# Optimization experiments

Measured on AMD Instinct MI355X. Metric: run time of the kernel, lower is better.

## Reference

```python
import jax, jax.numpy as jnp
import numpy as np

N, IN_DIM, HID = 8192, 256, 128


def _glorot(key, shape):
    lim = float(np.sqrt(6.0 / (shape[0] + shape[1])))
    return jax.random.uniform(key, shape, jnp.float32, -lim, lim)


def setup_inputs() -> dict:
    key = jax.random.key(0)
    ks = jax.random.split(key, 16)
    return {
        "x": jax.random.normal(ks[0], (N, IN_DIM), jnp.float32),
        "XY_Adj": jnp.zeros((N, N), jnp.float32),  # unused: overwritten by Cos_Adj in forward
        "w0": _glorot(ks[1], (IN_DIM, HID)),
        "w1": _glorot(ks[2], (IN_DIM, HID)),
        "Wq1": _glorot(ks[3], (IN_DIM, HID)), "bq1": jnp.zeros((HID,), jnp.float32),
        "Wk1": _glorot(ks[4], (IN_DIM, HID)), "bk1": jnp.zeros((HID,), jnp.float32),
        "Wv1": _glorot(ks[5], (IN_DIM, HID)), "bv1": jnp.zeros((HID,), jnp.float32),
        "Ws1": _glorot(ks[6], (IN_DIM, HID)), "bs1": jnp.zeros((HID,), jnp.float32),
        "Wq4": _glorot(ks[7], (HID, IN_DIM)), "bq4": jnp.zeros((IN_DIM,), jnp.float32),
        "Wk4": _glorot(ks[8], (HID, IN_DIM)), "bk4": jnp.zeros((IN_DIM,), jnp.float32),
        "Wv4": _glorot(ks[9], (HID, IN_DIM)), "bv4": jnp.zeros((IN_DIM,), jnp.float32),
        "Ws4": _glorot(ks[10], (HID, IN_DIM)), "bs4": jnp.zeros((IN_DIM,), jnp.float32),
    }


def _cos_adj(x, w0, w1):
    # Dense cosine-similarity adjacency, as in Cos_Adj.forward
    theta = x @ w0  # [N, HID]
    phi = x @ w1    # [N, HID]
    tn = jnp.linalg.norm(theta, axis=1, keepdims=True)  # [N,1]
    pn = jnp.linalg.norm(phi, axis=1, keepdims=True)    # [N,1]
    return (theta @ phi.T) / (tn @ pn.T + 1e-20)        # [N,N]


def _tconv(h, Wq, bq, Wk, bk, Wv, bv, Ws, bs):
    # PyG TransformerConv (heads=1, root_weight=True) on the fully-connected
    # graph produced by coo_matrix(sim_graph) == dense all-pairs attention.
    q = h @ Wq + bq
    k = h @ Wk + bk
    v = h @ Wv + bv
    scale = 1.0 / np.sqrt(q.shape[-1])
    attn = jax.nn.softmax((q @ k.T) * scale, axis=-1)  # [N,N]
    return attn @ v + (h @ Ws + bs)


def reference(x, XY_Adj, w0, w1,
              Wq1, bq1, Wk1, bk1, Wv1, bv1, Ws1, bs1,
              Wq4, bq4, Wk4, bk4, Wv4, bv4, Ws4, bs4):
    # Adjacency values only define the edge set (all N^2 pairs nonzero for
    # generic inputs); TransformerConv recomputes attention coefficients.
    sim = _cos_adj(x, w0, w1)  # noqa: F841 (edge set = nonzeros = all pairs)
    h1 = jax.nn.elu(_tconv(x, Wq1, bq1, Wk1, bk1, Wv1, bv1, Ws1, bs1))
    out = _tconv(h1, Wq4, bq4, Wk4, bk4, Wv4, bv4, Ws4, bs4)
    return out
```

## Files before the change

kernel.cpp:

```cpp
#include <hip/hip_runtime.h>

#define N_ROWS 8192
#define IN_DIM 256
#define HID 128

typedef __attribute__((ext_vector_type(8))) short bf16x8;
typedef __attribute__((ext_vector_type(4))) float f32x4;

__device__ __forceinline__ unsigned short f2bf(float f) {
    union { float f; unsigned u; } v; v.f = f;
    unsigned r = (v.u + 0x7FFFu + ((v.u >> 16) & 1u)) >> 16;
    return (unsigned short)r;
}

__global__ void pack_weights(const float* __restrict__ W0, const float* __restrict__ W1,
                             const float* __restrict__ W2, const float* __restrict__ W3,
                             const float* __restrict__ b0, const float* __restrict__ b1,
                             const float* __restrict__ b2, const float* __restrict__ b3,
                             unsigned short* __restrict__ WT, float* __restrict__ B,
                             int K, int HO)
{
    int NT = 4 * HO;
    int idx = blockIdx.x * blockDim.x + threadIdx.x;
    if (idx < NT * K) {
        int n = idx / K, k = idx - n * K;
        int s = n / HO, sn = n - s * HO;
        const float* W = (s == 0) ? W0 : (s == 1) ? W1 : (s == 2) ? W2 : W3;
        WT[idx] = f2bf(W[k * HO + sn]);
    }
    if (idx < NT) {
        int s = idx / HO, sn = idx - s * HO;
        const float* b = (s == 0) ? b0 : (s == 1) ? b1 : (s == 2) ? b2 : b3;
        B[idx] = b[sn];
    }
}

__global__ void cast_x(const float* __restrict__ in, unsigned short* __restrict__ out, int n) {
    int i = blockIdx.x * blockDim.x + threadIdx.x;
    if (i < n) out[i] = f2bf(in[i]);
}

__global__ void transpose_bf16(const unsigned short* __restrict__ in,
                               unsigned short* __restrict__ out, int R, int C)
{
    __shared__ unsigned short t[32][33];
    const int tx = threadIdx.x, ty = threadIdx.y;
    const int r0 = blockIdx.y * 32, c0 = blockIdx.x * 32;
    #pragma unroll
    for (int j = 0; j < 32; j += 8)
        t[ty + j][tx] = in[(size_t)(r0 + ty + j) * C + c0 + tx];
    __syncthreads();
    #pragma unroll
    for (int j = 0; j < 32; j += 8)
        out[(size_t)(c0 + ty + j) * R + r0 + tx] = t[tx][ty + j];
}

template<int K>
__global__ __launch_bounds__(256) void proj_gemm(
    const unsigned short* __restrict__ A, const unsigned short* __restrict__ WT,
    const float* __restrict__ bias,
    unsigned short* __restrict__ qo, unsigned short* __restrict__ ko,
    unsigned short* __restrict__ vo, float* __restrict__ skip,
    int NT, float qScale)
{
    const int lane = threadIdx.x & 63;
    const int wid = (blockIdx.x * blockDim.x + threadIdx.x) >> 6;
    const int nStrips = NT / 64;
    const int mTile = wid / nStrips;
    const int nBase = (wid - mTile * nStrips) * 64;
    const int l15 = lane & 15, lg = lane >> 4;
    const int HO = NT >> 2;

    f32x4 acc[4];
    #pragma unroll
    for (int c = 0; c < 4; ++c) acc[c] = f32x4{0.f, 0.f, 0.f, 0.f};

    const unsigned short* Ap = A + (size_t)(mTile * 16 + l15) * K + lg * 8;
    #pragma unroll
    for (int t = 0; t < K / 32; ++t) {
        bf16x8 a = *(const bf16x8*)(Ap + t * 32);
        #pragma unroll
        for (int c = 0; c < 4; ++c) {
            bf16x8 b = *(const bf16x8*)(WT + (size_t)(nBase + c * 16 + l15) * K + t * 32 + lg * 8);
            acc[c] = __builtin_amdgcn_mfma_f32_16x16x32_bf16(a, b, acc[c], 0, 0, 0);
        }
    }
    #pragma unroll
    for (int c = 0; c < 4; ++c) {
        int col = nBase + c * 16 + l15;
        int sec = col / HO, sc = col - sec * HO;
        float bv = bias[col];
        #pragma unroll
        for (int r = 0; r < 4; ++r) {
            int mrow = mTile * 16 + lg * 4 + r;
            float val = acc[c][r] + bv;
            size_t o = (size_t)mrow * HO + sc;
            if (sec == 0) qo[o] = f2bf(val * qScale);
            else if (sec == 1) ko[o] = f2bf(val);
            else if (sec == 2) vo[o] = f2bf(val);
            else skip[o] = val;
        }
    }
}

template<int D, int KB>
__global__ __launch_bounds__(512) void attn_partial(
    const unsigned short* __restrict__ Qm,
    const unsigned short* __restrict__ Km,
    const unsigned short* __restrict__ VTg,
    float* __restrict__ accOut, float* __restrict__ mOut, float* __restrict__ lOut,
    int chunkLen)
{
    constexpr int TPB = 512;
    constexpr int LK = D + 8;
    constexpr int LV = KB + 8;
    constexpr int LP = KB + 8;
    constexpr int DT = D / 16;
    static_assert(KB * D / 8 / TPB == 2, "two K staging int4s per thread");
    static_assert(D * KB / 8 / TPB == 2, "two V staging int4s per thread");
    __shared__ __align__(16) unsigned short Kl[KB * LK];
    __shared__ __align__(16) unsigned short VTl[(D + 16) * LV];
    __shared__ __align__(16) unsigned short Pl[8 * 16 * LP];

    const int tid = threadIdx.x;
    const int lane = tid & 63;
    const int w = tid >> 6;
    const int l15 = lane & 15, lg = lane >> 4;
    const int qrow = blockIdx.x * 128 + w * 16;
    const int kStart = blockIdx.y * chunkLen;
    const size_t NN = N_ROWS;

    const int kr0 = tid / (D / 8), kc0 = tid - kr0 * (D / 8);
    const int kr1 = (tid + TPB) / (D / 8), kc1 = (tid + TPB) - kr1 * (D / 8);
    const int kg0 = kr0 * D + kc0 * 8, kl0 = kr0 * LK + kc0 * 8;
    const int kg1 = kr1 * D + kc1 * 8, kl1 = kr1 * LK + kc1 * 8;
    const int vr0 = tid / (KB / 8), vc0 = tid - vr0 * (KB / 8);
    const int vr1 = (tid + TPB) / (KB / 8), vc1 = (tid + TPB) - vr1 * (KB / 8);
    const int vg0 = vr0 * (int)NN + vc0 * 8, vl0 = vr0 * LV + vc0 * 8;
    const int vg1 = vr1 * (int)NN + vc1 * 8, vl1 = vr1 * LV + vc1 * 8;

    for (int j = tid; j < 16 * LV; j += TPB) {
        int rr = j / LV, cc = j - rr * LV;
        VTl[(D + rr) * LV + cc] = (rr == 0) ? (unsigned short)0x3F80 : (unsigned short)0;
    }

    bf16x8 qf[D / 32];
    #pragma unroll
    for (int t = 0; t < D / 32; ++t)
        qf[t] = *(const bf16x8*)(Qm + (size_t)(qrow + l15) * D + t * 32 + lg * 8);

    f32x4 acc[DT + 1];
    #pragma unroll
    for (int dt = 0; dt <= DT; ++dt) acc[dt] = f32x4{0.f, 0.f, 0.f, 0.f};
    float mRow[4] = {-__builtin_inff(), -__builtin_inff(), -__builtin_inff(), -__builtin_inff()};

    const int nt = chunkLen / KB;
    const unsigned short* Kp = Km + (size_t)kStart * D;
    const unsigned short* Vp = VTg + kStart;
    int4 pk0 = *(const int4*)(Kp + kg0);
    int4 pk1 = *(const int4*)(Kp + kg1);
    int4 pv0 = *(const int4*)(Vp + vg0);
    int4 pv1 = *(const int4*)(Vp + vg1);

    for (int t = 0; t < nt; ++t) {
        __syncthreads();
        *(int4*)(&Kl[kl0]) = pk0;
        *(int4*)(&Kl[kl1]) = pk1;
        *(int4*)(&VTl[vl0]) = pv0;
        *(int4*)(&VTl[vl1]) = pv1;
        __syncthreads();
        if (t + 1 < nt) {
            const unsigned short* KpN = Kp + (size_t)(t + 1) * KB * D;
            const unsigned short* VpN = Vp + (t + 1) * KB;
            pk0 = *(const int4*)(KpN + kg0);
            pk1 = *(const int4*)(KpN + kg1);
            pv0 = *(const int4*)(VpN + vg0);
            pv1 = *(const int4*)(VpN + vg1);
        }
        f32x4 s[KB / 16];
        __builtin_amdgcn_s_setprio(1);
        #pragma unroll
        for (int c = 0; c < KB / 16; ++c) {
            s[c] = f32x4{0.f, 0.f, 0.f, 0.f};
            #pragma unroll
            for (int tt = 0; tt < D / 32; ++tt) {
                bf16x8 b = *(const bf16x8*)(&Kl[(c * 16 + l15) * LK + tt * 32 + lg * 8]);
                s[c] = __builtin_amdgcn_mfma_f32_16x16x32_bf16(qf[tt], b, s[c], 0, 0, 0);
            }
        }
        __builtin_amdgcn_s_setprio(0);
        float pm[4];
        #pragma unroll
        for (int r = 0; r < 4; ++r) {
            float v = s[0][r];
            #pragma unroll
            for (int c = 1; c < KB / 16; ++c) v = fmaxf(v, s[c][r]);
            pm[r] = v;
        }
        bool need = (pm[0] > mRow[0] + 8.f) || (pm[1] > mRow[1] + 8.f) ||
                    (pm[2] > mRow[2] + 8.f) || (pm[3] > mRow[3] + 8.f);
        if (__any(need)) {
            #pragma unroll
            for (int r = 0; r < 4; ++r) {
                float v = pm[r];
                #pragma unroll
                for (int mk = 1; mk <= 8; mk <<= 1) v = fmaxf(v, __shfl_xor(v, mk));
                float mN = fmaxf(mRow[r], v);
                float al = exp2f(mRow[r] - mN);
                mRow[r] = mN;
                #pragma unroll
                for (int dt = 0; dt <= DT; ++dt) acc[dt][r] *= al;
            }
        }
        #pragma unroll
        for (int c = 0; c < KB / 16; ++c) {
            #pragma unroll
            for (int r = 0; r < 4; ++r) {
                float p = exp2f(s[c][r] - mRow[r]);
                Pl[(w * 16 + lg * 4 + r) * LP + c * 16 + l15] = f2bf(p);
            }
        }
        __builtin_amdgcn_s_setprio(1);
        #pragma unroll
        for (int ks = 0; ks < KB / 32; ++ks) {
            bf16x8 a = *(const bf16x8*)(&Pl[(w * 16 + l15) * LP + ks * 32 + lg * 8]);
            #pragma unroll
            for (int dt = 0; dt <= DT; ++dt) {
                bf16x8 b = *(const bf16x8*)(&VTl[(dt * 16 + l15) * LV + ks * 32 + lg * 8]);
                acc[dt] = __builtin_amdgcn_mfma_f32_16x16x32_bf16(a, b, acc[dt], 0, 0, 0);
            }
        }
        __builtin_amdgcn_s_setprio(0);
    }

    #pragma unroll
    for (int dt = 0; dt < DT; ++dt)
        #pragma unroll
        for (int r = 0; r < 4; ++r)
            accOut[((size_t)blockIdx.y * NN + qrow + lg * 4 + r) * D + dt * 16 + l15] =
                acc[dt][r];
    if (l15 == 0) {
        #pragma unroll
        for (int r = 0; r < 4; ++r) {
            mOut[blockIdx.y * NN + qrow + lg * 4 + r] = mRow[r];
            lOut[blockIdx.y * NN + qrow + lg * 4 + r] = acc[DT][r];
        }
    }
}

template<int D, bool ELU>
__global__ void combine_kernel(const float* __restrict__ acc, const float* __restrict__ mArr,
                               const float* __restrict__ lArr, const float* __restrict__ skip,
                               float* __restrict__ outF, unsigned short* __restrict__ outB,
                               int CH)
{
    const int row = blockIdx.x;
    const int d = threadIdx.x;
    const size_t NN = N_ROWS;
    float mStar = -__builtin_inff();
    for (int c = 0; c < CH; ++c) mStar = fmaxf(mStar, mArr[c * NN + row]);
    float denom = 0.f, val = 0.f;
    for (int c = 0; c < CH; ++c) {
        float wgt = exp2f(mArr[c * NN + row] - mStar);
        denom += wgt * lArr[c * NN + row];
        val += wgt * acc[((size_t)c * NN + row) * D + d];
    }
    float v = val / denom + skip[(size_t)row * D + d];
    if (ELU) {
        v = (v > 0.f) ? v : expm1f(v);
        outB[(size_t)row * D + d] = f2bf(v);
    } else {
        outF[(size_t)row * D + d] = v;
    }
}

extern "C" void kernel_launch(void* const* d_in, const int* in_sizes, int n_in,
                              void* d_out, int out_size, void* d_ws, size_t ws_size,
                              hipStream_t stream)
{
    (void)in_sizes; (void)n_in; (void)out_size;
    const float* x   = (const float*)d_in[0];
    const float* Wq1 = (const float*)d_in[4];
    const float* bq1 = (const float*)d_in[5];
    const float* Wk1 = (const float*)d_in[6];
    const float* bk1 = (const float*)d_in[7];
    const float* Wv1 = (const float*)d_in[8];
    const float* bv1 = (const float*)d_in[9];
    const float* Ws1 = (const float*)d_in[10];
    const float* bs1 = (const float*)d_in[11];
    const float* Wq4 = (const float*)d_in[12];
    const float* bq4 = (const float*)d_in[13];
    const float* Wk4 = (const float*)d_in[14];
    const float* bk4 = (const float*)d_in[15];
    const float* Wv4 = (const float*)d_in[16];
    const float* bv4 = (const float*)d_in[17];
    const float* Ws4 = (const float*)d_in[18];
    const float* bs4 = (const float*)d_in[19];
    float* out = (float*)d_out;

    const int N = N_ROWS;
    size_t off = 0;
    auto alloc = [&](size_t bytes) -> void* {
        void* p = (char*)d_ws + off;
        off = (off + bytes + 255) & ~(size_t)255;
        return p;
    };
    unsigned short* xb  = (unsigned short*)alloc((size_t)N * IN_DIM * 2);
    unsigned short* WT1 = (unsigned short*)alloc((size_t)512 * 256 * 2);
    float* B1           = (float*)alloc(512 * 4);
    unsigned short* WT4 = (unsigned short*)alloc((size_t)1024 * 128 * 2);
    float* B4           = (float*)alloc(1024 * 4);
    unsigned short* q1  = (unsigned short*)alloc((size_t)N * HID * 2);
    unsigned short* k1  = (unsigned short*)alloc((size_t)N * HID * 2);
    unsigned short* v1  = (unsigned short*)alloc((size_t)N * HID * 2);
    unsigned short* VT1g= (unsigned short*)alloc((size_t)HID * N * 2);
    float* skip1        = (float*)alloc((size_t)N * HID * 4);
    unsigned short* h1  = (unsigned short*)alloc((size_t)N * HID * 2);
    unsigned short* q4  = (unsigned short*)alloc((size_t)N * IN_DIM * 2);
    unsigned short* k4  = (unsigned short*)alloc((size_t)N * IN_DIM * 2);
    unsigned short* v4  = (unsigned short*)alloc((size_t)N * IN_DIM * 2);
    unsigned short* VT4g= (unsigned short*)alloc((size_t)IN_DIM * N * 2);
    float* skip4        = (float*)alloc((size_t)N * IN_DIM * 4);

    size_t fixedEnd = off;
    size_t perCH = (size_t)N * 4 * 4 + (size_t)N * HID * 4 + (size_t)N * IN_DIM * 4 + 4096;
    int CH = 8;
    while (CH > 1 && fixedEnd + (size_t)CH * perCH > ws_size) CH >>= 1;

    float* m1   = (float*)alloc((size_t)CH * N * 4);
    float* l1   = (float*)alloc((size_t)CH * N * 4);
    float* m2   = (float*)alloc((size_t)CH * N * 4);
    float* l2   = (float*)alloc((size_t)CH * N * 4);
    float* acc1 = (float*)alloc((size_t)CH * N * HID * 4);
    float* acc2 = (float*)alloc((size_t)CH * N * IN_DIM * 4);
    if (off > ws_size && CH == 1) acc2 = out;

    const float LOG2E = 1.4426950408889634f;
    const float qs1 = 0.088388347648318447f * LOG2E;
    const float qs2 = 0.0625f * LOG2E;

    pack_weights<<<dim3((512 * 256 + 255) / 256), dim3(256), 0, stream>>>(
        Wq1, Wk1, Wv1, Ws1, bq1, bk1, bv1, bs1, WT1, B1, 256, 128);
    pack_weights<<<dim3((1024 * 128 + 255) / 256), dim3(256), 0, stream>>>(
        Wq4, Wk4, Wv4, Ws4, bq4, bk4, bv4, bs4, WT4, B4, 128, 256);
    cast_x<<<dim3((N * IN_DIM + 255) / 256), dim3(256), 0, stream>>>(x, xb, N * IN_DIM);

    proj_gemm<256><<<dim3((N / 16) * (512 / 64) / 4), dim3(256), 0, stream>>>(
        xb, WT1, B1, q1, k1, v1, skip1, 512, qs1);
    transpose_bf16<<<dim3(HID / 32, N / 32), dim3(32, 8), 0, stream>>>(v1, VT1g, N, HID);
    attn_partial<128, 64><<<dim3(N / 128, CH), dim3(512), 0, stream>>>(
        q1, k1, VT1g, acc1, m1, l1, N / CH);
    combine_kernel<128, true><<<dim3(N), dim3(128), 0, stream>>>(
        acc1, m1, l1, skip1, (float*)nullptr, h1, CH);

    proj_gemm<128><<<dim3((N / 16) * (1024 / 64) / 4), dim3(256), 0, stream>>>(
        h1, WT4, B4, q4, k4, v4, skip4, 1024, qs2);
    transpose_bf16<<<dim3(IN_DIM / 32, N / 32), dim3(32, 8), 0, stream>>>(v4, VT4g, N, IN_DIM);
    attn_partial<256, 32><<<dim3(N / 128, CH), dim3(512), 0, stream>>>(
        q4, k4, VT4g, acc2, m2, l2, N / CH);
    combine_kernel<256, false><<<dim3(N), dim3(256), 0, stream>>>(
        acc2, m2, l2, skip4, out, (unsigned short*)nullptr, CH);
}
```

Measured before the change: 287.5 us.

## Compute transposed attention scores to keep P in registers, dropping LDS round-trip

The QK^T MFMA is swapped to produce S^T so each lane holds scores for a single query row. This makes the row max a two-shuffle reduction, and the row sum is accumulated in a register instead of an extra ones-row MFMA tile. The probabilities are packed to bf16 with v_cvt_pk_bf16_f32 and rearranged across lanes with shuffles into the B-operand layout, which removes the Pl shared-memory buffer and its store/load traffic. Output stores become vectorized f32x4 writes. The tradeoffs are extra cross-lane shuffles and selects per step, plus a dependency on the exact MFMA register layout being correct.

After: 277.9 us. 1.03x faster.

```diff
diff --git a/kernel.cpp b/kernel.cpp
--- a/kernel.cpp
+++ b/kernel.cpp
@@ -11,6 +11,12 @@
     union { float f; unsigned u; } v; v.f = f;
     unsigned r = (v.u + 0x7FFFu + ((v.u >> 16) & 1u)) >> 16;
     return (unsigned short)r;
+}
+
+__device__ __forceinline__ unsigned cvt_pk_bf16(float lo, float hi) {
+    unsigned r;
+    asm("v_cvt_pk_bf16_f32 %0, %1, %2" : "=v"(r) : "v"(lo), "v"(hi));
+    return r;
 }
 
 __global__ void pack_weights(const float* __restrict__ W0, const float* __restrict__ W1,
@@ -114,13 +120,13 @@
     constexpr int TPB = 512;
     constexpr int LK = D + 8;
     constexpr int LV = KB + 8;
-    constexpr int LP = KB + 8;
     constexpr int DT = D / 16;
+    constexpr int CT = KB / 16;
+    constexpr int KS = KB / 32;
     static_assert(KB * D / 8 / TPB == 2, "two K staging int4s per thread");
     static_assert(D * KB / 8 / TPB == 2, "two V staging int4s per thread");
     __shared__ __align__(16) unsigned short Kl[KB * LK];
-    __shared__ __align__(16) unsigned short VTl[(D + 16) * LV];
-    __shared__ __align__(16) unsigned short Pl[8 * 16 * LP];
+    __shared__ __align__(16) unsigned short VTl[D * LV];
 
     const int tid = threadIdx.x;
     const int lane = tid & 63;
@@ -139,20 +145,16 @@
     const int vg0 = vr0 * (int)NN + vc0 * 8, vl0 = vr0 * LV + vc0 * 8;
     const int vg1 = vr1 * (int)NN + vc1 * 8, vl1 = vr1 * LV + vc1 * 8;
 
-    for (int j = tid; j < 16 * LV; j += TPB) {
-        int rr = j / LV, cc = j - rr * LV;
-        VTl[(D + rr) * LV + cc] = (rr == 0) ? (unsigned short)0x3F80 : (unsigned short)0;
-    }
-
     bf16x8 qf[D / 32];
     #pragma unroll
     for (int t = 0; t < D / 32; ++t)
         qf[t] = *(const bf16x8*)(Qm + (size_t)(qrow + l15) * D + t * 32 + lg * 8);
 
-    f32x4 acc[DT + 1];
-    #pragma unroll
-    for (int dt = 0; dt <= DT; ++dt) acc[dt] = f32x4{0.f, 0.f, 0.f, 0.f};
-    float mRow[4] = {-__builtin_inff(), -__builtin_inff(), -__builtin_inff(), -__builtin_inff()};
+    f32x4 acc[DT];
+    #pragma unroll
+    for (int dt = 0; dt < DT; ++dt) acc[dt] = f32x4{0.f, 0.f, 0.f, 0.f};
+    float mReg = -__builtin_inff();
+    float lReg = 0.f;
 
     const int nt = chunkLen / KB;
     const unsigned short* Kp = Km + (size_t)kStart * D;
@@ -177,74 +179,83 @@
             pv0 = *(const int4*)(VpN + vg0);
             pv1 = *(const int4*)(VpN + vg1);
         }
-        f32x4 s[KB / 16];
+        f32x4 sT[CT];
         __builtin_amdgcn_s_setprio(1);
         #pragma unroll
-        for (int c = 0; c < KB / 16; ++c) {
-            s[c] = f32x4{0.f, 0.f, 0.f, 0.f};
+        for (int c = 0; c < CT; ++c) {
+            sT[c] = f32x4{0.f, 0.f, 0.f, 0.f};
             #pragma unroll
             for (int tt = 0; tt < D / 32; ++tt) {
-                bf16x8 b = *(const bf16x8*)(&Kl[(c * 16 + l15) * LK + tt * 32 + lg * 8]);
-                s[c] = __builtin_amdgcn_mfma_f32_16x16x32_bf16(qf[tt], b, s[c], 0, 0, 0);
+                bf16x8 kf = *(const bf16x8*)(&Kl[(c * 16 + l15) * LK + tt * 32 + lg * 8]);
+                sT[c] = __builtin_amdgcn_mfma_f32_16x16x32_bf16(kf, qf[tt], sT[c], 0, 0, 0);
             }
         }
         __builtin_amdgcn_s_setprio(0);
-        float pm[4];
-        #pragma unroll
-        for (int r = 0; r < 4; ++r) {
-            float v = s[0][r];
+        float pmax = sT[0][0];
+        #pragma unroll
+        for (int c = 0; c < CT; ++c)
             #pragma unroll
-            for (int c = 1; c < KB / 16; ++c) v = fmaxf(v, s[c][r]);
-            pm[r] = v;
-        }
-        bool need = (pm[0] > mRow[0] + 8.f) || (pm[1] > mRow[1] + 8.f) ||
-                    (pm[2] > mRow[2] + 8.f) || (pm[3] > mRow[3] + 8.f);
+            for (int r = 0; r < 4; ++r) pmax = fmaxf(pmax, sT[c][r]);
+        bool need = pmax > mReg + 8.f;
         if (__any(need)) {
+            float v = pmax;
+            v = fmaxf(v, __shfl_xor(v, 16));
+            v = fmaxf(v, __shfl_xor(v, 32));
+            float mN = fmaxf(mReg, v);
+            float al = exp2f(mReg - mN);
+            mReg = mN;
+            lReg *= al;
             #pragma unroll
-            for (int r = 0; r < 4; ++r) {
-                float v = pm[r];
-                #pragma unroll
-                for (int mk = 1; mk <= 8; mk <<= 1) v = fmaxf(v, __shfl_xor(v, mk));
-                float mN = fmaxf(mRow[r], v);
-                float al = exp2f(mRow[r] - mN);
-                mRow[r] = mN;
-                #pragma unroll
-                for (int dt = 0; dt <= DT; ++dt) acc[dt][r] *= al;
+            for (int dt = 0; dt < DT; ++dt) acc[dt] *= al;
+        }
+        unsigned Wp[CT][2];
+        float lsum = 0.f;
+        #pragma unroll
+        for (int c = 0; c < CT; ++c) {
+            float p0 = exp2f(sT[c][0] - mReg);
+            float p1 = exp2f(sT[c][1] - mReg);
+            float p2 = exp2f(sT[c][2] - mReg);
+            float p3 = exp2f(sT[c][3] - mReg);
+            lsum += (p0 + p1) + (p2 + p3);
+            Wp[c][0] = cvt_pk_bf16(p0, p1);
+            Wp[c][1] = cvt_pk_bf16(p2, p3);
+        }
+        lReg += lsum;
+        #pragma unroll
+        for (int ks = 0; ks < KS; ++ks) {
+            unsigned x0 = Wp[2 * ks][0], x1 = Wp[2 * ks][1];
+            unsigned x2 = Wp[2 * ks + 1][0], x3 = Wp[2 * ks + 1][1];
+            const bool g1 = (lg & 2) != 0, g0 = (lg & 1) != 0;
+            unsigned s0 = g1 ? x0 : x2, s1 = g1 ? x1 : x3;
+            unsigned r0 = __shfl_xor(s0, 32), r1 = __shfl_xor(s1, 32);
+            unsigned k0 = g1 ? x2 : x0, k1 = g1 ? x3 : x1;
+            unsigned t0 = (g0 != g1) ? k0 : r0, t1 = (g0 != g1) ? k1 : r1;
+            unsigned q0 = __shfl_xor(t0, 16), q1 = __shfl_xor(t1, 16);
+            union { unsigned u[4]; bf16x8 v; } pb;
+            pb.u[0] = g0 ? q0 : (g1 ? r0 : k0);
+            pb.u[1] = g0 ? q1 : (g1 ? r1 : k1);
+            pb.u[2] = g0 ? (g1 ? k0 : r0) : q0;
+            pb.u[3] = g0 ? (g1 ? k1 : r1) : q1;
+            __builtin_amdgcn_s_setprio(1);
+            #pragma unroll
+            for (int dt = 0; dt < DT; ++dt) {
+                bf16x8 va = *(const bf16x8*)(&VTl[(dt * 16 + l15) * LV + ks * 32 + lg * 8]);
+                acc[dt] = __builtin_amdgcn_mfma_f32_16x16x32_bf16(va, pb.v, acc[dt], 0, 0, 0);
             }
-        }
-        #pragma unroll
-        for (int c = 0; c < KB / 16; ++c) {
-            #pragma unroll
-            for (int r = 0; r < 4; ++r) {
-                float p = exp2f(s[c][r] - mRow[r]);
-                Pl[(w * 16 + lg * 4 + r) * LP + c * 16 + l15] = f2bf(p);
-            }
-        }
-        __builtin_amdgcn_s_setprio(1);
-        #pragma unroll
-        for (int ks = 0; ks < KB / 32; ++ks) {
-            bf16x8 a = *(const bf16x8*)(&Pl[(w * 16 + l15) * LP + ks * 32 + lg * 8]);
-            #pragma unroll
-            for (int dt = 0; dt <= DT; ++dt) {
-                bf16x8 b = *(const bf16x8*)(&VTl[(dt * 16 + l15) * LV + ks * 32 + lg * 8]);
-                acc[dt] = __builtin_amdgcn_mfma_f32_16x16x32_bf16(a, b, acc[dt], 0, 0, 0);
-            }
-        }
-        __builtin_amdgcn_s_setprio(0);
-    }
-
+            __builtin_amdgcn_s_setprio(0);
+        }
+    }
+
+    lReg += __shfl_xor(lReg, 16);
+    lReg += __shfl_xor(lReg, 32);
+
+    float* accRow = accOut + ((size_t)blockIdx.y * NN + qrow + l15) * D + lg * 4;
     #pragma unroll
     for (int dt = 0; dt < DT; ++dt)
-        #pragma unroll
-        for (int r = 0; r < 4; ++r)
-            accOut[((size_t)blockIdx.y * NN + qrow + lg * 4 + r) * D + dt * 16 + l15] =
-                acc[dt][r];
-    if (l15 == 0) {
-        #pragma unroll
-        for (int r = 0; r < 4; ++r) {
-            mOut[blockIdx.y * NN + qrow + lg * 4 + r] = mRow[r];
-            lOut[blockIdx.y * NN + qrow + lg * 4 + r] = acc[DT][r];
-        }
+        *(f32x4*)(accRow + dt * 16) = acc[dt];
+    if (lg == 0) {
+        mOut[blockIdx.y * NN + qrow + l15] = mReg;
+        lOut[blockIdx.y * NN + qrow + l15] = lReg;
     }
 }
 
```
